# Optimization experiments

Measured on AMD Instinct MI355X. Metric: run time of the kernel, lower is better.

## Reference

```python
import jax, jax.numpy as jnp
import numpy as np

D_MODEL = 1024
NUM_HEADS = 16
D_HEAD = D_MODEL // NUM_HEADS
B, S = 4, 2048


def setup_inputs() -> dict:
    key = jax.random.key(0)
    ks = jax.random.split(key, 11)
    s = 1.0 / np.sqrt(D_MODEL)
    inp = {
        "query": jax.random.normal(ks[0], (B, S, D_MODEL), jnp.float32),
        "key": jax.random.normal(ks[1], (B, S, D_MODEL), jnp.float32),
        "value": jax.random.normal(ks[2], (B, S, D_MODEL), jnp.float32),
        "Wq": jax.random.uniform(ks[3], (D_MODEL, D_MODEL), jnp.float32, -s, s),
        "bq": jax.random.uniform(ks[4], (D_MODEL,), jnp.float32, -s, s),
        "Wk": jax.random.uniform(ks[5], (D_MODEL, D_MODEL), jnp.float32, -s, s),
        "bk": jax.random.uniform(ks[6], (D_MODEL,), jnp.float32, -s, s),
        "Wv": jax.random.uniform(ks[7], (D_MODEL, D_MODEL), jnp.float32, -s, s),
        "bv": jax.random.uniform(ks[8], (D_MODEL,), jnp.float32, -s, s),
        "Wo": jax.random.uniform(ks[9], (D_MODEL, D_MODEL), jnp.float32, -s, s),
        "bo": jax.random.uniform(ks[10], (D_MODEL,), jnp.float32, -s, s),
    }
    return inp


def reference(query, key, value, Wq, bq, Wk, bk, Wv, bv, Wo, bo):
    # Linear projections (torch Linear: x @ W.T + b)
    q = query @ Wq.T + bq  # [B,S,D]
    k = key @ Wk.T + bk
    v = value @ Wv.T + bv
    # split heads -> [B,H,S,Dh]
    def split(x):
        return x.reshape(B, S, NUM_HEADS, D_HEAD).transpose(0, 2, 1, 3)
    q, k, v = split(q), split(k), split(v)
    scale = 1.0 / np.sqrt(D_HEAD).astype(np.float32)
    scores = jnp.einsum('bhqd,bhkd->bhqk', q, k) * scale
    attn = jax.nn.softmax(scores, axis=-1)  # dropout is identity in eval
    ctx = jnp.einsum('bhqk,bhkd->bhqd', attn, v)
    ctx = ctx.transpose(0, 2, 1, 3).reshape(B, S, D_MODEL)
    return ctx @ Wo.T + bo
```

## Files before the change

kernel.cpp:

```cpp
#include <hip/hip_runtime.h>
#include <hip/hip_bf16.h>

typedef __bf16 bf16;
typedef bf16 bf16x8 __attribute__((ext_vector_type(8)));
typedef float f32x4 __attribute__((ext_vector_type(4)));
typedef float f32x16 __attribute__((ext_vector_type(16)));
typedef unsigned int u32x2 __attribute__((ext_vector_type(2)));
typedef unsigned int u32x4 __attribute__((ext_vector_type(4)));

#define B_  4
#define S_  2048
#define DM  1024
#define NH  16
#define DH  64

#define QSCALE 0.18033688011112042f


__device__ __forceinline__ void async_copy16(const void* g, void* lds) {
    __builtin_amdgcn_global_load_lds(
        (const __attribute__((address_space(1))) void*)g,
        (__attribute__((address_space(3))) void*)lds,
        16, 0, 0);
}

__device__ __forceinline__ bf16x8 read_frag(const char* lds, int row, int kbyte) {
    int off = row * 128 + (kbyte ^ ((row & 7) << 4));
    return *(const bf16x8*)(lds + off);
}

template<int ROWS, int NT>
__device__ __forceinline__ void stage_g2l(const bf16* g, int gs, char* lds) {
    int t = threadIdx.x;
#pragma unroll
    for (int i = 0; i < ROWS * 8 / NT; ++i) {
        int c = i * NT + t;
        int r = c >> 3;
        int s = (c & 7) ^ (r & 7);
        async_copy16(g + (long)r * gs + s * 8, lds + c * 16);
    }
}

__device__ __forceinline__ void stage_f32_g2l(const float* g, int gs, char* lds) {
    int t = threadIdx.x;
#pragma unroll
    for (int i = 0; i < 8; ++i) {
        int c = i * 256 + t;
        int r = c >> 4;
        int ch = c & 15;
        int sch = ch ^ (r & 15);
        async_copy16(g + (long)r * gs + sch * 4, lds + c * 16);
    }
}

__device__ __forceinline__ unsigned cvt_pk(float lo, float hi) {
    unsigned r;
    asm("v_cvt_pk_bf16_f32 %0, %1, %2" : "=v"(r) : "v"(lo), "v"(hi));
    return r;
}

__device__ __forceinline__ bf16x8 read_frag_f32(const char* lds, int row, int ks, int seg) {
    int ch0 = ks * 8 + seg * 2;
    int sw = row & 15;
    const char* base = lds + row * 256;
    f32x4 lo = *(const f32x4*)(base + ((ch0 ^ sw) * 16));
    f32x4 hi = *(const f32x4*)(base + (((ch0 + 1) ^ sw) * 16));
    u32x4 w;
    w.x = cvt_pk(lo[0], lo[1]);
    w.y = cvt_pk(lo[2], lo[3]);
    w.z = cvt_pk(hi[0], hi[1]);
    w.w = cvt_pk(hi[2], hi[3]);
    return __builtin_bit_cast(bf16x8, w);
}

__device__ __forceinline__ u32x2 pl32swap(unsigned a, unsigned b) {
    return __builtin_amdgcn_permlane32_swap(a, b, false, false);
}


__device__ __forceinline__ void cvt_body(const float* __restrict__ s, bf16* __restrict__ d, int n8) {
    for (int i = blockIdx.x * 256 + threadIdx.x; i < n8; i += gridDim.x * 256) {
        f32x4 v0 = *(const f32x4*)(s + (long)i * 8);
        f32x4 v1 = *(const f32x4*)(s + (long)i * 8 + 4);
        bf16x8 r;
#pragma unroll
        for (int j = 0; j < 4; ++j) { r[j] = (bf16)v0[j]; r[j + 4] = (bf16)v1[j]; }
        *(bf16x8*)(d + (long)i * 8) = r;
    }
}

__global__ __launch_bounds__(256) void cvt_w(
    const float* __restrict__ a, const float* __restrict__ b,
    const float* __restrict__ c, const float* __restrict__ d,
    bf16* __restrict__ oa, bf16* __restrict__ ob, bf16* __restrict__ oc, bf16* __restrict__ od)
{
    int z = blockIdx.y;
    cvt_body(z == 0 ? a : z == 1 ? b : z == 2 ? c : d,
             z == 0 ? oa : z == 1 ? ob : z == 2 ? oc : od, DM * DM / 8);
}

__global__ __launch_bounds__(256) void qkv_gemm(
    const float* __restrict__ xq, const float* __restrict__ xk, const float* __restrict__ xv,
    const bf16* __restrict__ wq, const bf16* __restrict__ wk, const bf16* __restrict__ wv,
    const float* __restrict__ bq, const float* __restrict__ bk, const float* __restrict__ bv,
    bf16* __restrict__ qo, bf16* __restrict__ ko, bf16* __restrict__ vo)
{
    __shared__ alignas(128) char As[128 * 256];
    __shared__ alignas(128) char Bs[128 * 128];

    int z = blockIdx.y;
    const float* X    = (z == 0) ? xq : (z == 1) ? xk : xv;
    const bf16* W     = (z == 0) ? wq : (z == 1) ? wk : wv;
    const float* bias = (z == 0) ? bq : (z == 1) ? bk : bv;
    bf16* out         = (z == 0) ? qo : (z == 1) ? ko : vo;
    float scale       = (z == 0) ? QSCALE : 1.0f;
    bool  vt          = (z == 2);

    int p = blockIdx.x;
    int xcd = p & 7, slot = p >> 3;
    int m0 = (xcd * 8 + (slot >> 3)) * 128;
    int n0 = (slot & 7) * 128;

    int lane = threadIdx.x & 63, wid = threadIdx.x >> 6;
    int wm = (wid >> 1) * 64, wn = (wid & 1) * 64;
    int seg = lane >> 4;

    f32x4 acc[4][4];
#pragma unroll
    for (int i = 0; i < 4; ++i)
#pragma unroll
        for (int j = 0; j < 4; ++j) acc[i][j] = f32x4{0.f, 0.f, 0.f, 0.f};

    for (int k0 = 0; k0 < DM; k0 += 64) {
        __syncthreads();
        stage_f32_g2l(X + (long)m0 * DM + k0, DM, As);
        stage_g2l<128, 256>(W + (long)n0 * DM + k0, DM, Bs);
        __syncthreads();
#pragma unroll
        for (int ks = 0; ks < 2; ++ks) {
            int kb = ks * 64 + seg * 16;
            bf16x8 af[4], bfr[4];
#pragma unroll
            for (int f = 0; f < 4; ++f)
                af[f] = read_frag_f32(As, wm + f * 16 + (lane & 15), ks, seg);
#pragma unroll
            for (int f = 0; f < 4; ++f)
                bfr[f] = read_frag(Bs, wn + f * 16 + (lane & 15), kb);
#pragma unroll
            for (int mf = 0; mf < 4; ++mf)
#pragma unroll
                for (int nf = 0; nf < 4; ++nf)
                    acc[mf][nf] = __builtin_amdgcn_mfma_f32_16x16x32_bf16(
                        af[mf], bfr[nf], acc[mf][nf], 0, 0, 0);
        }
    }

#pragma unroll
    for (int nf = 0; nf < 4; ++nf) {
        int j = n0 + wn + nf * 16 + (lane & 15);
        float bj = bias[j];
        int h = j >> 6, dh = j & 63;
#pragma unroll
        for (int mf = 0; mf < 4; ++mf) {
#pragma unroll
            for (int r = 0; r < 4; ++r) {
                int i = m0 + wm + mf * 16 + (lane >> 4) * 4 + r;
                float v = (acc[mf][nf][r] + bj) * scale;
                int b = i >> 11, s = i & 2047;
                long addr = vt ? ((long)((b * NH + h) * DH + dh)) * S_ + s
                               : ((long)((b * NH + h) * S_ + s)) * DH + dh;
                out[addr] = (bf16)v;
            }
        }
    }
}

__global__ __launch_bounds__(256) void out_gemm(
    const bf16* __restrict__ ctxb, const bf16* __restrict__ wo, const float* __restrict__ bo,
    float* __restrict__ out)
{
    __shared__ alignas(128) char As[128 * 128];
    __shared__ alignas(128) char Bs[128 * 128];

    int p = blockIdx.x;
    int xcd = p & 7, slot = p >> 3;
    int m0 = (xcd * 8 + (slot >> 3)) * 128;
    int n0 = (slot & 7) * 128;

    int lane = threadIdx.x & 63, wid = threadIdx.x >> 6;
    int wm = (wid >> 1) * 64, wn = (wid & 1) * 64;

    f32x4 acc[4][4];
#pragma unroll
    for (int i = 0; i < 4; ++i)
#pragma unroll
        for (int j = 0; j < 4; ++j) acc[i][j] = f32x4{0.f, 0.f, 0.f, 0.f};

    for (int k0 = 0; k0 < DM; k0 += 64) {
        __syncthreads();
        stage_g2l<128, 256>(ctxb + (long)m0 * DM + k0, DM, As);
        stage_g2l<128, 256>(wo + (long)n0 * DM + k0, DM, Bs);
        __syncthreads();
#pragma unroll
        for (int ks = 0; ks < 2; ++ks) {
            int kb = ks * 64 + (lane >> 4) * 16;
            bf16x8 af[4], bfr[4];
#pragma unroll
            for (int f = 0; f < 4; ++f) af[f]  = read_frag(As, wm + f * 16 + (lane & 15), kb);
#pragma unroll
            for (int f = 0; f < 4; ++f) bfr[f] = read_frag(Bs, wn + f * 16 + (lane & 15), kb);
#pragma unroll
            for (int mf = 0; mf < 4; ++mf)
#pragma unroll
                for (int nf = 0; nf < 4; ++nf)
                    acc[mf][nf] = __builtin_amdgcn_mfma_f32_16x16x32_bf16(
                        af[mf], bfr[nf], acc[mf][nf], 0, 0, 0);
        }
    }

#pragma unroll
    for (int nf = 0; nf < 4; ++nf) {
        int j = n0 + wn + nf * 16 + (lane & 15);
        float bj = bo[j];
#pragma unroll
        for (int mf = 0; mf < 4; ++mf)
#pragma unroll
            for (int r = 0; r < 4; ++r) {
                int i = m0 + wm + mf * 16 + (lane >> 4) * 4 + r;
                out[(long)i * DM + j] = acc[mf][nf][r] + bj;
            }
    }
}

__global__ __launch_bounds__(256) void attn_fwd(
    const bf16* __restrict__ qb, const bf16* __restrict__ kb, const bf16* __restrict__ vtb,
    bf16* __restrict__ ctx)
{
    __shared__ alignas(128) char Ks[2][64 * 128];
    __shared__ alignas(128) char Vs[2][64 * 128];

    int bid = blockIdx.x;
    int xcd = bid & 7, rest = bid >> 3;
    int qt = rest & 15, bh = xcd + 8 * (rest >> 4);

    int lane = threadIdx.x & 63, wid = threadIdx.x >> 6;
    int ln = lane & 31, h = lane >> 5;
    int q0w = qt * 128 + wid * 32;

    const bf16* qg = qb + (long)bh * S_ * DH;
    const bf16* kg = kb + (long)bh * S_ * DH;
    const bf16* vg = vtb + (long)bh * DH * S_;

    bf16x8 qf[4];
#pragma unroll
    for (int s = 0; s < 4; ++s)
        qf[s] = *(const bf16x8*)(qg + (long)(q0w + ln) * DH + s * 16 + h * 8);

    const bf16x8 onea = __builtin_bit_cast(bf16x8,
        u32x4{0x3F803F80u, 0x3F803F80u, 0x3F803F80u, 0x3F803F80u});

    f32x16 fz;
#pragma unroll
    for (int r = 0; r < 16; ++r) fz[r] = 0.f;

    f32x16 o[2];
#pragma unroll
    for (int t = 0; t < 2; ++t)
#pragma unroll
        for (int r = 0; r < 16; ++r) o[t][r] = 0.f;
    f32x16 lacc;
#pragma unroll
    for (int r = 0; r < 16; ++r) lacc[r] = 0.f;

    stage_g2l<64, 256>(kg, DH, Ks[0]);
    stage_g2l<64, 256>(vg, S_, Vs[0]);
    __syncthreads();
    stage_g2l<64, 256>(kg + (long)64 * DH, DH, Ks[1]);
    stage_g2l<64, 256>(vg + 64, S_, Vs[1]);

    f32x16 acc2[2];
    __builtin_amdgcn_s_setprio(1);
#pragma unroll
    for (int t = 0; t < 2; ++t) {
        bf16x8 ka = read_frag(Ks[0], 32 * t + ln, 16 * h);
        acc2[t] = __builtin_amdgcn_mfma_f32_32x32x16_bf16(ka, qf[0], fz, 0, 0, 0);
    }
#pragma unroll
    for (int s = 1; s < 4; ++s)
#pragma unroll
        for (int t = 0; t < 2; ++t) {
            bf16x8 ka = read_frag(Ks[0], 32 * t + ln, 32 * s + 16 * h);
            acc2[t] = __builtin_amdgcn_mfma_f32_32x32x16_bf16(ka, qf[s], acc2[t], 0, 0, 0);
        }
    __builtin_amdgcn_s_setprio(0);

    unsigned pf[4][4];
#pragma unroll
    for (int t = 0; t < 2; ++t)
#pragma unroll
        for (int r = 0; r < 16; ++r)
            acc2[t][r] = __builtin_amdgcn_exp2f(acc2[t][r]);
#pragma unroll
    for (int t = 0; t < 2; ++t)
#pragma unroll
        for (int hf = 0; hf < 2; ++hf) {
            int rb = 8 * hf;
            unsigned a0 = cvt_pk(acc2[t][rb + 0], acc2[t][rb + 1]);
            unsigned s0 = cvt_pk(acc2[t][rb + 4], acc2[t][rb + 5]);
            unsigned a1 = cvt_pk(acc2[t][rb + 2], acc2[t][rb + 3]);
            unsigned s1 = cvt_pk(acc2[t][rb + 6], acc2[t][rb + 7]);
            u32x2 r0 = pl32swap(a0, s0);
            u32x2 r1 = pl32swap(a1, s1);
            int kt = 2 * t + hf;
            pf[kt][0] = r0.x; pf[kt][2] = r0.y;
            pf[kt][1] = r1.x; pf[kt][3] = r1.y;
        }

    const int NT = S_ / 64;
    for (int t = 0; t < NT; ++t) {
        int cur = t & 1, nxt = cur ^ 1;
        __syncthreads();

        __builtin_amdgcn_s_setprio(1);
        if (t + 1 < NT) {
#pragma unroll
            for (int tt = 0; tt < 2; ++tt) {
                bf16x8 ka = read_frag(Ks[nxt], 32 * tt + ln, 16 * h);
                acc2[tt] = __builtin_amdgcn_mfma_f32_32x32x16_bf16(ka, qf[0], fz, 0, 0, 0);
            }
#pragma unroll
            for (int s = 1; s < 4; ++s)
#pragma unroll
                for (int tt = 0; tt < 2; ++tt) {
                    bf16x8 ka = read_frag(Ks[nxt], 32 * tt + ln, 32 * s + 16 * h);
                    acc2[tt] = __builtin_amdgcn_mfma_f32_32x32x16_bf16(ka, qf[s], acc2[tt], 0, 0, 0);
                }
        }
#pragma unroll
        for (int kt = 0; kt < 4; ++kt) {
            bf16x8 pb = __builtin_bit_cast(bf16x8,
                u32x4{pf[kt][0], pf[kt][1], pf[kt][2], pf[kt][3]});
            bf16x8 va0 = read_frag(Vs[cur], ln,      32 * kt + 16 * h);
            o[0] = __builtin_amdgcn_mfma_f32_32x32x16_bf16(va0, pb, o[0], 0, 0, 0);
            bf16x8 va1 = read_frag(Vs[cur], 32 + ln, 32 * kt + 16 * h);
            o[1] = __builtin_amdgcn_mfma_f32_32x32x16_bf16(va1, pb, o[1], 0, 0, 0);
            lacc = __builtin_amdgcn_mfma_f32_32x32x16_bf16(onea, pb, lacc, 0, 0, 0);
        }
        __builtin_amdgcn_s_setprio(0);

        __syncthreads();

        if (t + 2 < NT) {
            stage_g2l<64, 256>(kg + (long)(t + 2) * 64 * DH, DH, Ks[cur]);
            stage_g2l<64, 256>(vg + (t + 2) * 64, S_, Vs[cur]);
        }

        if (t + 1 < NT) {
#pragma unroll
            for (int tt = 0; tt < 2; ++tt)
#pragma unroll
                for (int r = 0; r < 16; ++r)
                    acc2[tt][r] = __builtin_amdgcn_exp2f(acc2[tt][r]);
#pragma unroll
            for (int tt = 0; tt < 2; ++tt)
#pragma unroll
                for (int hf = 0; hf < 2; ++hf) {
                    int rb = 8 * hf;
                    unsigned a0 = cvt_pk(acc2[tt][rb + 0], acc2[tt][rb + 1]);
                    unsigned s0 = cvt_pk(acc2[tt][rb + 4], acc2[tt][rb + 5]);
                    unsigned a1 = cvt_pk(acc2[tt][rb + 2], acc2[tt][rb + 3]);
                    unsigned s1 = cvt_pk(acc2[tt][rb + 6], acc2[tt][rb + 7]);
                    u32x2 r0 = pl32swap(a0, s0);
                    u32x2 r1 = pl32swap(a1, s1);
                    int kt = 2 * tt + hf;
                    pf[kt][0] = r0.x; pf[kt][2] = r0.y;
                    pf[kt][1] = r1.x; pf[kt][3] = r1.y;
                }
        }
    }

    int b = bh >> 4, head = bh & 15;
    float inv = 1.0f / lacc[0];
    int s = q0w + ln;
    bf16* base = ctx + ((long)(b * S_ + s)) * DM + head * DH;
#pragma unroll
    for (int dt = 0; dt < 2; ++dt)
#pragma unroll
        for (int c = 0; c < 4; ++c) {
            int d0 = 32 * dt + 8 * c + 4 * h;
            u32x2 st;
            st.x = cvt_pk(o[dt][4 * c + 0] * inv, o[dt][4 * c + 1] * inv);
            st.y = cvt_pk(o[dt][4 * c + 2] * inv, o[dt][4 * c + 3] * inv);
            *(u32x2*)(base + d0) = st;
        }
}

extern "C" void kernel_launch(void* const* d_in, const int* in_sizes, int n_in,
                              void* d_out, int out_size, void* d_ws, size_t ws_size,
                              hipStream_t stream) {
    const float* query = (const float*)d_in[0];
    const float* key   = (const float*)d_in[1];
    const float* value = (const float*)d_in[2];
    const float* Wq = (const float*)d_in[3];
    const float* bq = (const float*)d_in[4];
    const float* Wk = (const float*)d_in[5];
    const float* bk = (const float*)d_in[6];
    const float* Wv = (const float*)d_in[7];
    const float* bv = (const float*)d_in[8];
    const float* Wo = (const float*)d_in[9];
    const float* bo = (const float*)d_in[10];
    float* out = (float*)d_out;

    char* ws = (char*)d_ws;
    const long MB = 1ll << 20;
    bf16* qb   = (bf16*)(ws + 0 * MB);
    bf16* kb   = (bf16*)(ws + 16 * MB);
    bf16* vtb  = (bf16*)(ws + 32 * MB);
    bf16* ctxb = (bf16*)(ws + 48 * MB);
    bf16* wqb  = (bf16*)(ws + 64 * MB);
    bf16* wkb  = (bf16*)(ws + 66 * MB);
    bf16* wvb  = (bf16*)(ws + 68 * MB);
    bf16* wob  = (bf16*)(ws + 70 * MB);

    dim3 blk(256);
    cvt_w<<<dim3(512, 4), blk, 0, stream>>>(Wq, Wk, Wv, Wo, wqb, wkb, wvb, wob);
    qkv_gemm<<<dim3(512, 3), blk, 0, stream>>>(query, key, value, wqb, wkb, wvb,
                                               bq, bk, bv, qb, kb, vtb);
    attn_fwd<<<dim3(1024), blk, 0, stream>>>(qb, kb, vtb, ctxb);
    out_gemm<<<dim3(512), blk, 0, stream>>>(ctxb, wob, bo, out);
}
```

Before: 209.4 us.

## Use partial vmcnt waits and raw barriers to keep next tile's loads in flight

Replaces the full __syncthreads (which drains all outstanding global-to-LDS loads) with s_waitcnt vmcnt(4) plus s_barrier, so the prefetch of tile t+2 can stay in flight while tile t+1 is consumed. It also moves the QK^T MFMA for the next tile from before the PV MFMAs to after the stage/barrier point, changing the order of work within each iteration. This aims to overlap memory latency with compute better. It relies on the hand-counted vmcnt matching the number of async copies issued per stage, which is fragile if the staging helper changes.

New measurement: 214.3 us. 1.02x slower.

```diff
diff --git a/kernel.cpp b/kernel.cpp
--- a/kernel.cpp
+++ b/kernel.cpp
@@ -274,68 +274,54 @@
 
     stage_g2l<64, 256>(kg, DH, Ks[0]);
     stage_g2l<64, 256>(vg, S_, Vs[0]);
-    __syncthreads();
     stage_g2l<64, 256>(kg + (long)64 * DH, DH, Ks[1]);
     stage_g2l<64, 256>(vg + 64, S_, Vs[1]);
+    asm volatile("s_waitcnt vmcnt(4)" ::: "memory");
+    __builtin_amdgcn_s_barrier();
+    __builtin_amdgcn_sched_barrier(0);
 
     f32x16 acc2[2];
+    unsigned pf[4][4];
     __builtin_amdgcn_s_setprio(1);
 #pragma unroll
-    for (int t = 0; t < 2; ++t) {
-        bf16x8 ka = read_frag(Ks[0], 32 * t + ln, 16 * h);
-        acc2[t] = __builtin_amdgcn_mfma_f32_32x32x16_bf16(ka, qf[0], fz, 0, 0, 0);
+    for (int tt = 0; tt < 2; ++tt) {
+        bf16x8 ka = read_frag(Ks[0], 32 * tt + ln, 16 * h);
+        acc2[tt] = __builtin_amdgcn_mfma_f32_32x32x16_bf16(ka, qf[0], fz, 0, 0, 0);
     }
 #pragma unroll
     for (int s = 1; s < 4; ++s)
 #pragma unroll
-        for (int t = 0; t < 2; ++t) {
-            bf16x8 ka = read_frag(Ks[0], 32 * t + ln, 32 * s + 16 * h);
-            acc2[t] = __builtin_amdgcn_mfma_f32_32x32x16_bf16(ka, qf[s], acc2[t], 0, 0, 0);
+        for (int tt = 0; tt < 2; ++tt) {
+            bf16x8 ka = read_frag(Ks[0], 32 * tt + ln, 32 * s + 16 * h);
+            acc2[tt] = __builtin_amdgcn_mfma_f32_32x32x16_bf16(ka, qf[s], acc2[tt], 0, 0, 0);
         }
     __builtin_amdgcn_s_setprio(0);
-
-    unsigned pf[4][4];
-#pragma unroll
-    for (int t = 0; t < 2; ++t)
+#pragma unroll
+    for (int tt = 0; tt < 2; ++tt)
 #pragma unroll
         for (int r = 0; r < 16; ++r)
-            acc2[t][r] = __builtin_amdgcn_exp2f(acc2[t][r]);
-#pragma unroll
-    for (int t = 0; t < 2; ++t)
+            acc2[tt][r] = __builtin_amdgcn_exp2f(acc2[tt][r]);
+#pragma unroll
+    for (int tt = 0; tt < 2; ++tt)
 #pragma unroll
         for (int hf = 0; hf < 2; ++hf) {
             int rb = 8 * hf;
-            unsigned a0 = cvt_pk(acc2[t][rb + 0], acc2[t][rb + 1]);
-            unsigned s0 = cvt_pk(acc2[t][rb + 4], acc2[t][rb + 5]);
-            unsigned a1 = cvt_pk(acc2[t][rb + 2], acc2[t][rb + 3]);
-            unsigned s1 = cvt_pk(acc2[t][rb + 6], acc2[t][rb + 7]);
+            unsigned a0 = cvt_pk(acc2[tt][rb + 0], acc2[tt][rb + 1]);
+            unsigned s0 = cvt_pk(acc2[tt][rb + 4], acc2[tt][rb + 5]);
+            unsigned a1 = cvt_pk(acc2[tt][rb + 2], acc2[tt][rb + 3]);
+            unsigned s1 = cvt_pk(acc2[tt][rb + 6], acc2[tt][rb + 7]);
             u32x2 r0 = pl32swap(a0, s0);
             u32x2 r1 = pl32swap(a1, s1);
-            int kt = 2 * t + hf;
+            int kt = 2 * tt + hf;
             pf[kt][0] = r0.x; pf[kt][2] = r0.y;
             pf[kt][1] = r1.x; pf[kt][3] = r1.y;
         }
 
     const int NT = S_ / 64;
     for (int t = 0; t < NT; ++t) {
-        int cur = t & 1, nxt = cur ^ 1;
-        __syncthreads();
+        int cur = t & 1;
 
         __builtin_amdgcn_s_setprio(1);
-        if (t + 1 < NT) {
-#pragma unroll
-            for (int tt = 0; tt < 2; ++tt) {
-                bf16x8 ka = read_frag(Ks[nxt], 32 * tt + ln, 16 * h);
-                acc2[tt] = __builtin_amdgcn_mfma_f32_32x32x16_bf16(ka, qf[0], fz, 0, 0, 0);
-            }
-#pragma unroll
-            for (int s = 1; s < 4; ++s)
-#pragma unroll
-                for (int tt = 0; tt < 2; ++tt) {
-                    bf16x8 ka = read_frag(Ks[nxt], 32 * tt + ln, 32 * s + 16 * h);
-                    acc2[tt] = __builtin_amdgcn_mfma_f32_32x32x16_bf16(ka, qf[s], acc2[tt], 0, 0, 0);
-                }
-        }
 #pragma unroll
         for (int kt = 0; kt < 4; ++kt) {
             bf16x8 pb = __builtin_bit_cast(bf16x8,
@@ -348,14 +334,37 @@
         }
         __builtin_amdgcn_s_setprio(0);
 
-        __syncthreads();
+        asm volatile("" ::: "memory");
+        __builtin_amdgcn_s_barrier();
+        asm volatile("" ::: "memory");
 
         if (t + 2 < NT) {
             stage_g2l<64, 256>(kg + (long)(t + 2) * 64 * DH, DH, Ks[cur]);
             stage_g2l<64, 256>(vg + (t + 2) * 64, S_, Vs[cur]);
-        }
+            asm volatile("s_waitcnt vmcnt(4)" ::: "memory");
+        } else {
+            asm volatile("s_waitcnt vmcnt(0)" ::: "memory");
+        }
+        __builtin_amdgcn_s_barrier();
+        __builtin_amdgcn_sched_barrier(0);
 
         if (t + 1 < NT) {
+            int nxt = cur ^ 1;
+            __builtin_amdgcn_s_setprio(1);
+#pragma unroll
+            for (int tt = 0; tt < 2; ++tt) {
+                bf16x8 ka = read_frag(Ks[nxt], 32 * tt + ln, 16 * h);
+                acc2[tt] = __builtin_amdgcn_mfma_f32_32x32x16_bf16(ka, qf[0], fz, 0, 0, 0);
+            }
+#pragma unroll
+            for (int s = 1; s < 4; ++s)
+#pragma unroll
+                for (int tt = 0; tt < 2; ++tt) {
+                    bf16x8 ka = read_frag(Ks[nxt], 32 * tt + ln, 32 * s + 16 * h);
+                    acc2[tt] = __builtin_amdgcn_mfma_f32_32x32x16_bf16(ka, qf[s], acc2[tt], 0, 0, 0);
+                }
+            __builtin_amdgcn_s_setprio(0);
+
 #pragma unroll
             for (int tt = 0; tt < 2; ++tt)
 #pragma unroll
```

## Double-buffer QKV projection GEMM with async LDS prefetch and 32-wide K steps

Applied to the files above, without the earlier changes.

Restructures the QKV projection main loop from single-buffered 64-wide K tiles into double-buffered 32-wide K tiles. The next tile's global-to-LDS async copies are issued while the current tile is computed, and partial vmcnt waits let loads overlap MFMA work. It also adds s_setprio around the MFMA block and uses new swizzle patterns for the narrower tiles. The cost is more barriers per K step (32 iterations instead of 16), and the correctness of the hand-written waitcnt counts depends on how the compiler orders the loads.

Result: no change. 210.1 us (+0.3%).

```diff
diff --git a/kernel.cpp b/kernel.cpp
--- a/kernel.cpp
+++ b/kernel.cpp
@@ -41,30 +41,42 @@
     }
 }
 
-__device__ __forceinline__ void stage_f32_g2l(const float* g, int gs, char* lds) {
-    int t = threadIdx.x;
-#pragma unroll
-    for (int i = 0; i < 8; ++i) {
-        int c = i * 256 + t;
-        int r = c >> 4;
-        int ch = c & 15;
-        int sch = ch ^ (r & 15);
-        async_copy16(g + (long)r * gs + sch * 4, lds + c * 16);
-    }
-}
-
 __device__ __forceinline__ unsigned cvt_pk(float lo, float hi) {
     unsigned r;
     asm("v_cvt_pk_bf16_f32 %0, %1, %2" : "=v"(r) : "v"(lo), "v"(hi));
     return r;
 }
 
-__device__ __forceinline__ bf16x8 read_frag_f32(const char* lds, int row, int ks, int seg) {
-    int ch0 = ks * 8 + seg * 2;
-    int sw = row & 15;
-    const char* base = lds + row * 256;
-    f32x4 lo = *(const f32x4*)(base + ((ch0 ^ sw) * 16));
-    f32x4 hi = *(const f32x4*)(base + (((ch0 + 1) ^ sw) * 16));
+__device__ __forceinline__ u32x2 pl32swap(unsigned a, unsigned b) {
+    return __builtin_amdgcn_permlane32_swap(a, b, false, false);
+}
+
+__device__ __forceinline__ void stage_a32(const float* g, int gs, char* lds) {
+    int t = threadIdx.x;
+#pragma unroll
+    for (int i = 0; i < 4; ++i) {
+        int c = i * 256 + t;
+        int r = c >> 3;
+        int sch = (c & 7) ^ (r & 7);
+        async_copy16(g + (long)r * gs + sch * 4, lds + c * 16);
+    }
+}
+__device__ __forceinline__ void stage_b32(const bf16* g, int gs, char* lds) {
+    int t = threadIdx.x;
+#pragma unroll
+    for (int i = 0; i < 2; ++i) {
+        int c = i * 256 + t;
+        int r = c >> 2;
+        int sch = (c & 3) ^ ((r >> 1) & 3);
+        async_copy16(g + (long)r * gs + sch * 8, lds + c * 16);
+    }
+}
+
+__device__ __forceinline__ bf16x8 read_a32(const char* lds, int row, int seg) {
+    int sw = row & 7;
+    const char* base = lds + row * 128;
+    f32x4 lo = *(const f32x4*)(base + (((seg * 2) ^ sw) * 16));
+    f32x4 hi = *(const f32x4*)(base + (((seg * 2 + 1) ^ sw) * 16));
     u32x4 w;
     w.x = cvt_pk(lo[0], lo[1]);
     w.y = cvt_pk(lo[2], lo[3]);
@@ -72,9 +84,9 @@
     w.w = cvt_pk(hi[2], hi[3]);
     return __builtin_bit_cast(bf16x8, w);
 }
-
-__device__ __forceinline__ u32x2 pl32swap(unsigned a, unsigned b) {
-    return __builtin_amdgcn_permlane32_swap(a, b, false, false);
+__device__ __forceinline__ bf16x8 read_b32(const char* lds, int row, int seg) {
+    int off = row * 64 + ((seg ^ ((row >> 1) & 3)) * 16);
+    return *(const bf16x8*)(lds + off);
 }
 
 
@@ -105,8 +117,11 @@
     const float* __restrict__ bq, const float* __restrict__ bk, const float* __restrict__ bv,
     bf16* __restrict__ qo, bf16* __restrict__ ko, bf16* __restrict__ vo)
 {
-    __shared__ alignas(128) char As[128 * 256];
-    __shared__ alignas(128) char Bs[128 * 128];
+    __shared__ alignas(128) char lds[49152];
+    char* A0 = lds;
+    char* A1 = lds + 16384;
+    char* B0 = lds + 32768;
+    char* B1 = lds + 40960;
 
     int z = blockIdx.y;
     const float* X    = (z == 0) ? xq : (z == 1) ? xk : xv;
@@ -125,34 +140,57 @@
     int wm = (wid >> 1) * 64, wn = (wid & 1) * 64;
     int seg = lane >> 4;
 
+    const float* Xb = X + (long)m0 * DM;
+    const bf16*  Wb = W + (long)n0 * DM;
+
     f32x4 acc[4][4];
 #pragma unroll
     for (int i = 0; i < 4; ++i)
 #pragma unroll
         for (int j = 0; j < 4; ++j) acc[i][j] = f32x4{0.f, 0.f, 0.f, 0.f};
 
-    for (int k0 = 0; k0 < DM; k0 += 64) {
-        __syncthreads();
-        stage_f32_g2l(X + (long)m0 * DM + k0, DM, As);
-        stage_g2l<128, 256>(W + (long)n0 * DM + k0, DM, Bs);
-        __syncthreads();
-#pragma unroll
-        for (int ks = 0; ks < 2; ++ks) {
-            int kb = ks * 64 + seg * 16;
-            bf16x8 af[4], bfr[4];
-#pragma unroll
-            for (int f = 0; f < 4; ++f)
-                af[f] = read_frag_f32(As, wm + f * 16 + (lane & 15), ks, seg);
-#pragma unroll
-            for (int f = 0; f < 4; ++f)
-                bfr[f] = read_frag(Bs, wn + f * 16 + (lane & 15), kb);
-#pragma unroll
-            for (int mf = 0; mf < 4; ++mf)
-#pragma unroll
-                for (int nf = 0; nf < 4; ++nf)
-                    acc[mf][nf] = __builtin_amdgcn_mfma_f32_16x16x32_bf16(
-                        af[mf], bfr[nf], acc[mf][nf], 0, 0, 0);
-        }
+    stage_a32(Xb,      DM, A0);  stage_b32(Wb,      DM, B0);
+    stage_a32(Xb + 32, DM, A1);  stage_b32(Wb + 32, DM, B1);
+    asm volatile("s_waitcnt vmcnt(6)" ::: "memory");
+    __builtin_amdgcn_s_barrier();
+    __builtin_amdgcn_sched_barrier(0);
+
+    for (int k = 0; k < 32; ++k) {
+        const char* Ab = (k & 1) ? A1 : A0;
+        const char* Bb = (k & 1) ? B1 : B0;
+
+        bf16x8 af[4], bfr[4];
+#pragma unroll
+        for (int f = 0; f < 4; ++f)
+            af[f] = read_a32(Ab, wm + f * 16 + (lane & 15), seg);
+#pragma unroll
+        for (int f = 0; f < 4; ++f)
+            bfr[f] = read_b32(Bb, wn + f * 16 + (lane & 15), seg);
+
+        __builtin_amdgcn_s_setprio(1);
+#pragma unroll
+        for (int mf = 0; mf < 4; ++mf)
+#pragma unroll
+            for (int nf = 0; nf < 4; ++nf)
+                acc[mf][nf] = __builtin_amdgcn_mfma_f32_16x16x32_bf16(
+                    af[mf], bfr[nf], acc[mf][nf], 0, 0, 0);
+        __builtin_amdgcn_s_setprio(0);
+
+        asm volatile("" ::: "memory");
+        __builtin_amdgcn_s_barrier();
+        asm volatile("" ::: "memory");
+
+        if (k + 2 < 32) {
+            char* An = (k & 1) ? A1 : A0;
+            char* Bn = (k & 1) ? B1 : B0;
+            stage_a32(Xb + (k + 2) * 32, DM, An);
+            stage_b32(Wb + (k + 2) * 32, DM, Bn);
+            asm volatile("s_waitcnt vmcnt(6)" ::: "memory");
+        } else {
+            asm volatile("s_waitcnt vmcnt(0)" ::: "memory");
+        }
+        __builtin_amdgcn_s_barrier();
+        __builtin_amdgcn_sched_barrier(0);
     }
 
 #pragma unroll
```
